# Performance work log

Hardware: AMD Instinct MI355X
Metric: run time of the kernel (lower is better)

Reference implementation:

```python
import jax, jax.numpy as jnp
import numpy as np

NUM_NODES = 50000
NUM_OBS = 800000


def graph_conv(x, src, dst, ew, W_rel, b_rel, W_root):
    # PyG GraphConv: out[i] = lin_rel(sum_{j->i} e * x[j]) + lin_root(x[i])
    msg = x[src] * ew[:, None]                         # [E, d_in] gather + weight
    agg = jax.ops.segment_sum(msg, dst, num_segments=NUM_NODES)  # scatter-add
    return agg @ W_rel + b_rel + x @ W_root


def setup_inputs() -> dict:
    key = jax.random.key(0)
    ks = jax.random.split(key, 16)
    E = 2 * NUM_OBS
    def lin(k, i, o):
        return jax.random.normal(k, (i, o), jnp.float32) / np.sqrt(i)
    return {
        "x": jax.random.normal(ks[0], (NUM_NODES, 2), jnp.float32),
        "edge_index": jax.random.randint(ks[1], (2, E), 0, NUM_NODES, jnp.int32),
        "edge_weight_norm": jax.random.uniform(ks[2], (E,), jnp.float32),
        "num_obs": NUM_OBS,
        "W1_rel": lin(ks[3], 2, 128), "b1": jnp.zeros((128,), jnp.float32),
        "W1_root": lin(ks[4], 2, 128),
        "W2_rel": lin(ks[5], 128, 64), "b2": jnp.zeros((64,), jnp.float32),
        "W2_root": lin(ks[6], 128, 64),
        "W3_rel": lin(ks[7], 64, 64), "b3": jnp.zeros((64,), jnp.float32),
        "W3_root": lin(ks[8], 64, 64),
        "dec_W1": lin(ks[9], 128, 128), "dec_b1": jnp.zeros((128,), jnp.float32),
        "dec_W2": lin(ks[10], 128, 1), "dec_b2": jnp.zeros((1,), jnp.float32),
    }


def reference(x, edge_index, edge_weight_norm, num_obs,
              W1_rel, b1, W1_root, W2_rel, b2, W2_root, W3_rel, b3, W3_root,
              dec_W1, dec_b1, dec_W2, dec_b2):
    src, dst = edge_index[0], edge_index[1]
    # encoder (eval mode: dropout is identity)
    h = jax.nn.relu(graph_conv(x, src, dst, edge_weight_norm, W1_rel, b1, W1_root))
    h = jax.nn.relu(graph_conv(h, src, dst, edge_weight_norm, W2_rel, b2, W2_root))
    z = graph_conv(h, src, dst, edge_weight_norm, W3_rel, b3, W3_root)
    # decoder over the first num_obs edges
    s = src[:num_obs]
    d = dst[:num_obs]
    h_cat = jnp.concatenate([z[s], z[d]], axis=1)      # [num_obs, 2*latent]
    pred = (jax.nn.relu(h_cat @ dec_W1 + dec_b1) @ dec_W2 + dec_b2)[:, 0]
    # pred_full[:num_obs] = pred; pred_full[num_obs:2*num_obs] = pred
    pred_full = jnp.concatenate([pred, pred], axis=0)
    return pred_full, z
```

## Files before the change

kernel.cpp:

```cpp
#include <hip/hip_runtime.h>
#include <hip/hip_bf16.h>

static inline int cdiv(long long a, long long b) { return (int)((a + b - 1) / b); }

__device__ inline float bf_lo(unsigned u) { return __uint_as_float(u << 16); }
__device__ inline float bf_hi(unsigned u) { return __uint_as_float(u & 0xffff0000u); }

typedef short bf16x8 __attribute__((ext_vector_type(8)));
typedef float f32x4 __attribute__((ext_vector_type(4)));

#define CHUNK 8192

__global__ __launch_bounds__(256) void prep_weights_kernel(
    const float* __restrict__ W2rel, const float* __restrict__ W2rt,
    const float* __restrict__ W3rel, const float* __restrict__ W3rt,
    const float* __restrict__ dW1, __hip_bfloat16* __restrict__ wt)
{
    int i = blockIdx.x * 256 + threadIdx.x;
    if (i >= 40960) return;
    float v;
    if (i < 8192)       { int n = i >> 7, k = i & 127;              v = W2rel[k * 64 + n]; }
    else if (i < 16384) { int j = i - 8192;  int n = j >> 7, k = j & 127; v = W2rt[k * 64 + n]; }
    else if (i < 20480) { int j = i - 16384; int n = j >> 6, k = j & 63;  v = W3rel[k * 64 + n]; }
    else if (i < 24576) { int j = i - 20480; int n = j >> 6, k = j & 63;  v = W3rt[k * 64 + n]; }
    else if (i < 32768) { int j = i - 24576; int n = j >> 6, k = j & 63;  v = dW1[k * 128 + n]; }
    else                { int j = i - 32768; int n = j >> 6, k = j & 63;  v = dW1[(64 + k) * 128 + n]; }
    wt[i] = __float2bfloat16(v);
}

template <int K, int NOUT, int EPI>
__global__ __launch_bounds__(256) void mfma_gemm_kernel(
    const __hip_bfloat16* __restrict__ A,
    const __hip_bfloat16* __restrict__ Wt,
    const float* __restrict__ bias,
    const float* __restrict__ extra,
    __hip_bfloat16* __restrict__ outb,
    float* __restrict__ outf, int M)
{
    constexpr int KF = K / 32;
    constexpr int SPW = NOUT / 64;
    const int wv = threadIdx.x >> 6;
    const int lane = threadIdx.x & 63;
    const int m = lane & 15, q = lane >> 4;
    const int row0 = blockIdx.x * 16;
    const int arow = row0 + m;

    bf16x8 af[KF];
    #pragma unroll
    for (int kf = 0; kf < KF; kf++)
        af[kf] = *(const bf16x8*)(A + (size_t)arow * K + kf * 32 + q * 8);

    #pragma unroll
    for (int s = 0; s < SPW; s++) {
        const int col = (wv * SPW + s) * 16 + m;
        f32x4 acc = {0.f, 0.f, 0.f, 0.f};
        #pragma unroll
        for (int kf = 0; kf < KF; kf++) {
            bf16x8 bf = *(const bf16x8*)(Wt + (size_t)col * K + kf * 32 + q * 8);
            acc = __builtin_amdgcn_mfma_f32_16x16x32_bf16(af[kf], bf, acc, 0, 0, 0);
        }
        #pragma unroll
        for (int r = 0; r < 4; r++) {
            int rr = row0 + q * 4 + r;
            size_t idx = (size_t)rr * NOUT + col;
            float v = acc[r];
            if (EPI >= 1) v += extra[idx] + bias[col];
            if (EPI == 1) v = fmaxf(v, 0.f);
            if (EPI == 2) outf[idx] = v;
            outb[idx] = __float2bfloat16(v);
        }
    }
}


__global__ __launch_bounds__(256) void p1_hist_kernel(
    const int* __restrict__ dst, int* __restrict__ ghist,
    int E, int nchunks, int nb)
{
    __shared__ int sh[512];
    int c = blockIdx.x;
    for (int i = threadIdx.x; i < nb; i += 256) sh[i] = 0;
    __syncthreads();
    int base = c * CHUNK;
    int end = min(base + CHUNK, E);
    for (int i = base + threadIdx.x; i < end; i += 256)
        atomicAdd(&sh[dst[i] >> 7], 1);
    __syncthreads();
    for (int i = threadIdx.x; i < nb; i += 256)
        ghist[i * nchunks + c] = sh[i];
}

__global__ __launch_bounds__(256) void p2_scatter_kernel(
    const int* __restrict__ src, const int* __restrict__ dst,
    const float* __restrict__ ew, const int* __restrict__ gs,
    uint2* __restrict__ bpos, int E, int nchunks, int nb)
{
    __shared__ int cur[512];
    int c = blockIdx.x;
    for (int i = threadIdx.x; i < nb; i += 256) cur[i] = gs[i * nchunks + c];
    __syncthreads();
    int base = c * CHUNK;
    int end = min(base + CHUNK, E);
    for (int i = base + threadIdx.x; i < end; i += 256) {
        int d = dst[i];
        int pos = atomicAdd(&cur[d >> 7], 1);
        bpos[pos] = make_uint2(((unsigned)d << 16) | (unsigned)src[i],
                               __float_as_uint(ew[i]));
    }
}

__global__ __launch_bounds__(256) void p3_place_kernel(
    const uint2* __restrict__ bpos, const int* __restrict__ gs,
    int* __restrict__ deg, int* __restrict__ off,
    float2* __restrict__ csr, int E, int nchunks, int nb, int N)
{
    __shared__ int cnt[128];
    __shared__ int pos[128];
    int b = blockIdx.x;
    int nodebase = b << 7;
    if (threadIdx.x < 128) cnt[threadIdx.x] = 0;
    __syncthreads();
    int begin = gs[b * nchunks];
    int bend = (b + 1 < nb) ? gs[(b + 1) * nchunks] : E;
    for (int i = begin + threadIdx.x; i < bend; i += 256)
        atomicAdd(&cnt[(bpos[i].x >> 16) - nodebase], 1);
    __syncthreads();
    int v = 0;
    if (threadIdx.x < 128) { v = cnt[threadIdx.x]; pos[threadIdx.x] = v; }
    __syncthreads();
    #pragma unroll
    for (int ofs = 1; ofs < 128; ofs <<= 1) {
        int t = 0;
        if (threadIdx.x < 128 && threadIdx.x >= ofs) t = pos[threadIdx.x - ofs];
        __syncthreads();
        if (threadIdx.x < 128) pos[threadIdx.x] += t;
        __syncthreads();
    }
    if (threadIdx.x < 128) {
        int ex = begin + pos[threadIdx.x] - v;
        int n = nodebase + threadIdx.x;
        if (n < N) { off[n] = ex; deg[n] = v; }
        cnt[threadIdx.x] = ex;
    }
    __syncthreads();
    for (int i = begin + threadIdx.x; i < bend; i += 256) {
        uint2 en = bpos[i];
        int d = en.x >> 16;
        int p = atomicAdd(&cnt[d - nodebase], 1);
        csr[p] = make_float2(__int_as_float((int)(en.x & 0xffffu)),
                             __uint_as_float(en.y));
    }
}


__global__ __launch_bounds__(1024) void scan_block_kernel(
    const int* __restrict__ in, int* __restrict__ out,
    int* __restrict__ partials, int N)
{
    __shared__ int sdata[1024];
    const int tid = threadIdx.x;
    const int i = blockIdx.x * 1024 + tid;
    int v = (i < N) ? in[i] : 0;
    sdata[tid] = v;
    __syncthreads();
    #pragma unroll
    for (int ofs = 1; ofs < 1024; ofs <<= 1) {
        int t = (tid >= ofs) ? sdata[tid - ofs] : 0;
        __syncthreads();
        sdata[tid] += t;
        __syncthreads();
    }
    if (i < N) out[i] = sdata[tid] - v;
    if (partials && tid == 1023) partials[blockIdx.x] = sdata[1023];
}

__global__ __launch_bounds__(1024) void scan_add_kernel(
    int* __restrict__ off, const int* __restrict__ blockoff, int N)
{
    int i = blockIdx.x * blockDim.x + threadIdx.x;
    if (i < N) off[i] += blockoff[i >> 10];
}


__global__ __launch_bounds__(256) void hist_kernel(
    const int* __restrict__ dst, int* __restrict__ deg, int E)
{
    int e = blockIdx.x * blockDim.x + threadIdx.x;
    if (e < E) atomicAdd(&deg[dst[e]], 1);
}

__global__ __launch_bounds__(256) void fill_csr_kernel(
    const int* __restrict__ src, const int* __restrict__ dst,
    const float* __restrict__ ew, const int* __restrict__ off,
    int* __restrict__ cursor, float2* __restrict__ csr, int E)
{
    int e = blockIdx.x * blockDim.x + threadIdx.x;
    if (e >= E) return;
    int d = dst[e];
    int i = off[d] + atomicAdd(&cursor[d], 1);
    csr[i] = make_float2(__int_as_float(src[e]), ew[e]);
}


__global__ __launch_bounds__(256) void layer1_fused_kernel(
    const float2* __restrict__ x2, const float2* __restrict__ csr,
    const int* __restrict__ off, const int* __restrict__ deg,
    const float* __restrict__ W1rel, const float* __restrict__ W1rt,
    const float* __restrict__ b1, __hip_bfloat16* __restrict__ h1b, int N)
{
    int t = blockIdx.x * blockDim.x + threadIdx.x;
    int n = t >> 6;
    if (n >= N) return;
    int lane = t & 63;
    int beg = off[n], cnt = deg[n];
    float a0 = 0.f, a1 = 0.f;
    for (int i = lane; i < cnt; i += 64) {
        float2 c = csr[beg + i];
        float2 xs = x2[__float_as_int(c.x)];
        a0 = fmaf(c.y, xs.x, a0);
        a1 = fmaf(c.y, xs.y, a1);
    }
    #pragma unroll
    for (int o = 32; o > 0; o >>= 1) {
        a0 += __shfl_xor(a0, o, 64);
        a1 += __shfl_xor(a1, o, 64);
    }
    float2 xn = x2[n];
    float v0 = b1[lane] + a0 * W1rel[lane] + a1 * W1rel[128 + lane]
             + xn.x * W1rt[lane] + xn.y * W1rt[128 + lane];
    float v1 = b1[64 + lane] + a0 * W1rel[64 + lane] + a1 * W1rel[192 + lane]
             + xn.x * W1rt[64 + lane] + xn.y * W1rt[192 + lane];
    h1b[(size_t)n * 128 + lane]      = __float2bfloat16(fmaxf(v0, 0.f));
    h1b[(size_t)n * 128 + 64 + lane] = __float2bfloat16(fmaxf(v1, 0.f));
}


__global__ __launch_bounds__(256) void gather_b16_kernel(
    const float2* __restrict__ csr, const int* __restrict__ off,
    const int* __restrict__ deg, const __hip_bfloat162* __restrict__ p,
    float* __restrict__ agg, int N)
{
    int t = blockIdx.x * blockDim.x + threadIdx.x;
    int n = t >> 6;
    if (n >= N) return;
    int lane = t & 63;
    int half = lane >> 5;
    int fp = lane & 31;
    int beg = off[n], cnt = deg[n];
    float a0 = 0.f, a1 = 0.f;
    int i = half;
    for (; i + 2 < cnt; i += 4) {
        float2 c0 = csr[beg + i];
        float2 c1 = csr[beg + i + 2];
        float2 v0 = __bfloat1622float2(p[(size_t)__float_as_int(c0.x) * 32 + fp]);
        float2 v1 = __bfloat1622float2(p[(size_t)__float_as_int(c1.x) * 32 + fp]);
        a0 = fmaf(c0.y, v0.x, a0); a1 = fmaf(c0.y, v0.y, a1);
        a0 = fmaf(c1.y, v1.x, a0); a1 = fmaf(c1.y, v1.y, a1);
    }
    for (; i < cnt; i += 2) {
        float2 c = csr[beg + i];
        float2 v = __bfloat1622float2(p[(size_t)__float_as_int(c.x) * 32 + fp]);
        a0 = fmaf(c.y, v.x, a0); a1 = fmaf(c.y, v.y, a1);
    }
    a0 += __shfl_xor(a0, 32, 64);
    a1 += __shfl_xor(a1, 32, 64);
    if (half == 0)
        ((float2*)agg)[(size_t)n * 32 + fp] = make_float2(a0, a1);
}


__global__ __launch_bounds__(256) void scatter_f64_kernel(
    const int* __restrict__ src, const int* __restrict__ dst,
    const float* __restrict__ ew, const float* __restrict__ p,
    float* __restrict__ agg, int E)
{
    int t = blockIdx.x * blockDim.x + threadIdx.x;
    int e = t >> 6;
    if (e >= E) return;
    int j = t & 63;
    atomicAdd(&agg[(size_t)dst[e] * 64 + j], p[(size_t)src[e] * 64 + j] * ew[e]);
}

__global__ __launch_bounds__(256) void scatter_f2_kernel(
    const int* __restrict__ src, const int* __restrict__ dst,
    const float* __restrict__ ew, const float* __restrict__ x,
    float* __restrict__ agg, int E)
{
    int e = blockIdx.x * blockDim.x + threadIdx.x;
    if (e >= E) return;
    int s = src[e], d = dst[e];
    float w = ew[e];
    atomicAdd(&agg[d * 2 + 0], x[s * 2 + 0] * w);
    atomicAdd(&agg[d * 2 + 1], x[s * 2 + 1] * w);
}

__global__ __launch_bounds__(256) void layer1_kernel(
    const float* __restrict__ x, const float* __restrict__ agg,
    const float* __restrict__ W1rel, const float* __restrict__ W1root,
    const float* __restrict__ b1, float* __restrict__ h1, int N)
{
    int t = blockIdx.x * blockDim.x + threadIdx.x;
    if (t >= N * 128) return;
    int n = t >> 7, j = t & 127;
    float v = b1[j]
        + agg[n * 2 + 0] * W1rel[j] + agg[n * 2 + 1] * W1rel[128 + j]
        + x[n * 2 + 0] * W1root[j] + x[n * 2 + 1] * W1root[128 + j];
    h1[t] = fmaxf(v, 0.f);
}

template <int K, int NOUT, bool RELU, bool HAS_EXTRA, bool HAS_BIAS, bool OUT_BF16>
__global__ __launch_bounds__(256) void gemm_small(
    const float* __restrict__ in, int M,
    const float* __restrict__ W, int ldw, int woff,
    const float* __restrict__ bias,
    const float* __restrict__ extra,
    void* __restrict__ out_)
{
    constexpr int CPT = NOUT / 64;
    __shared__ float sW[K * NOUT];
    __shared__ float sX[4][K];
    const int tid = threadIdx.x;
    const int lane = tid & 63;
    const int wv = tid >> 6;
    for (int idx = tid; idx < K * NOUT; idx += 256) {
        int k = idx / NOUT;
        int j = idx - k * NOUT;
        sW[idx] = W[(size_t)(k + woff) * ldw + j];
    }
    __syncthreads();
    const int ROWS = 32;
    int r0 = blockIdx.x * ROWS;
    for (int rr = wv; rr < ROWS; rr += 4) {
        int r = r0 + rr;
        if (r >= M) break;
        #pragma unroll
        for (int kk = lane; kk < K; kk += 64) sX[wv][kk] = in[(size_t)r * K + kk];
        float acc[CPT][4];
        #pragma unroll
        for (int c = 0; c < CPT; c++)
            #pragma unroll
            for (int u = 0; u < 4; u++) acc[c][u] = 0.f;
        #pragma unroll
        for (int k = 0; k < K; k += 4) {
            #pragma unroll
            for (int u = 0; u < 4; u++) {
                float xv = sX[wv][k + u];
                #pragma unroll
                for (int c = 0; c < CPT; c++)
                    acc[c][u] = fmaf(xv, sW[(k + u) * NOUT + c * 64 + lane], acc[c][u]);
            }
        }
        #pragma unroll
        for (int c = 0; c < CPT; c++) {
            float v = (acc[c][0] + acc[c][1]) + (acc[c][2] + acc[c][3]);
            int j = c * 64 + lane;
            if (HAS_EXTRA) v += extra[(size_t)r * NOUT + j];
            if (HAS_BIAS) v += bias[j];
            if (RELU) v = fmaxf(v, 0.f);
            if (OUT_BF16)
                ((__hip_bfloat16*)out_)[(size_t)r * NOUT + j] = __float2bfloat16(v);
            else
                ((float*)out_)[(size_t)r * NOUT + j] = v;
        }
    }
}


__global__ __launch_bounds__(256) void decoder16_kernel(
    const int* __restrict__ src, const int* __restrict__ dst,
    const uint4* __restrict__ Za, const uint4* __restrict__ Zb,
    const float* __restrict__ db1, const float* __restrict__ dW2,
    const float* __restrict__ db2, float* __restrict__ pred,
    int Eobs, int nseg)
{
    int t = blockIdx.x * blockDim.x + threadIdx.x;
    int l = t & 15;
    int seg = t >> 4;
    float4 c1a = ((const float4*)db1)[2 * l];
    float4 c1b = ((const float4*)db1)[2 * l + 1];
    float4 w2a = ((const float4*)dW2)[2 * l];
    float4 w2b = ((const float4*)dW2)[2 * l + 1];
    float b2v = db2[0];

    for (int e = seg; e < Eobs; e += nseg) {
        int s = src[e], d = dst[e];
        uint4 ua = Za[(size_t)s * 16 + l];
        uint4 ub = Zb[(size_t)d * 16 + l];
        float acc;
        acc  = fmaxf(bf_lo(ua.x) + bf_lo(ub.x) + c1a.x, 0.f) * w2a.x;
        acc += fmaxf(bf_hi(ua.x) + bf_hi(ub.x) + c1a.y, 0.f) * w2a.y;
        acc += fmaxf(bf_lo(ua.y) + bf_lo(ub.y) + c1a.z, 0.f) * w2a.z;
        acc += fmaxf(bf_hi(ua.y) + bf_hi(ub.y) + c1a.w, 0.f) * w2a.w;
        acc += fmaxf(bf_lo(ua.z) + bf_lo(ub.z) + c1b.x, 0.f) * w2b.x;
        acc += fmaxf(bf_hi(ua.z) + bf_hi(ub.z) + c1b.y, 0.f) * w2b.y;
        acc += fmaxf(bf_lo(ua.w) + bf_lo(ub.w) + c1b.z, 0.f) * w2b.z;
        acc += fmaxf(bf_hi(ua.w) + bf_hi(ub.w) + c1b.w, 0.f) * w2b.w;
        #pragma unroll
        for (int o = 8; o > 0; o >>= 1) acc += __shfl_xor(acc, o, 64);
        if (l == 0) {
            float pv = acc + b2v;
            pred[e] = pv;
            pred[e + Eobs] = pv;
        }
    }
}

__global__ __launch_bounds__(256) void decoder_kernel(
    const int* __restrict__ src, const int* __restrict__ dst,
    const float* __restrict__ Z1a, const float* __restrict__ Z1b,
    const float* __restrict__ db1, const float* __restrict__ dW2,
    const float* __restrict__ db2, float* __restrict__ pred, int Eobs)
{
    int t = blockIdx.x * blockDim.x + threadIdx.x;
    int e = t >> 6;
    if (e >= Eobs) return;
    int lane = threadIdx.x & 63;
    int s = src[e], d = dst[e];
    float t0 = Z1a[(size_t)s * 128 + lane] + Z1b[(size_t)d * 128 + lane] + db1[lane];
    float t1 = Z1a[(size_t)s * 128 + lane + 64] + Z1b[(size_t)d * 128 + lane + 64] + db1[lane + 64];
    t0 = fmaxf(t0, 0.f);
    t1 = fmaxf(t1, 0.f);
    float acc = t0 * dW2[lane] + t1 * dW2[lane + 64];
    #pragma unroll
    for (int off = 32; off > 0; off >>= 1) acc += __shfl_xor(acc, off, 64);
    if (lane == 0) {
        float pv = acc + db2[0];
        pred[e] = pv;
        pred[e + Eobs] = pv;
    }
}


extern "C" void kernel_launch(void* const* d_in, const int* in_sizes, int n_in,
                              void* d_out, int out_size, void* d_ws, size_t ws_size,
                              hipStream_t stream)
{
    const float* x     = (const float*)d_in[0];
    const int*   ei    = (const int*)d_in[1];
    const float* ew    = (const float*)d_in[2];
    const float* W1rel = (const float*)d_in[4];
    const float* b1    = (const float*)d_in[5];
    const float* W1rt  = (const float*)d_in[6];
    const float* W2rel = (const float*)d_in[7];
    const float* b2    = (const float*)d_in[8];
    const float* W2rt  = (const float*)d_in[9];
    const float* W3rel = (const float*)d_in[10];
    const float* b3    = (const float*)d_in[11];
    const float* W3rt  = (const float*)d_in[12];
    const float* dW1   = (const float*)d_in[13];
    const float* db1   = (const float*)d_in[14];
    const float* dW2   = (const float*)d_in[15];
    const float* db2   = (const float*)d_in[16];

    const int E    = in_sizes[2];
    const int N    = in_sizes[0] / 2;
    const int Eobs = E / 2;
    const int* src = ei;
    const int* dst = ei + E;

    float* agg  = (float*)d_ws;
    float* R1   = agg + (size_t)N * 64;
    float* R2   = R1 + (size_t)N * 64;
    float* R3   = R2 + (size_t)N * 32;
    float* R4   = R3 + (size_t)N * 32;
    int*   deg  = (int*)(R4 + (size_t)N * 64);
    int*   off  = deg + N;
    int*   par1 = off + N;
    int*   par2 = par1 + 1024;
    float* wtf  = (float*)(par2 + 1024);
    __hip_bfloat16* wt = (__hip_bfloat16*)wtf;
    float2* csr = (float2*)(wtf + 20480);

    __hip_bfloat16* h1b   = (__hip_bfloat16*)R1;
    __hip_bfloat16* Z1a16 = (__hip_bfloat16*)R1;
    __hip_bfloat16* pb16  = (__hip_bfloat16*)R2;
    __hip_bfloat16* zb16  = (__hip_bfloat16*)R2;
    __hip_bfloat16* h2b   = (__hip_bfloat16*)R3;
    __hip_bfloat16* Z1b16 = (__hip_bfloat16*)R4;
    uint2* bpos  = (uint2*)R4;
    int*   ghist = (int*)agg;

    const int nb      = (N + 127) >> 7;
    const int nchunks = cdiv(E, CHUNK);
    const int M       = nb * nchunks;
    int* ghist_s = ghist + M;

    size_t need = ((size_t)N * 258 + 22528 + (size_t)E * 2) * 4;
    const bool fast = (ws_size >= need) && nb <= 512 && N <= 65535 &&
                      (N % 16 == 0) &&
                      (size_t)E * 2 <= (size_t)N * 64 &&
                      (size_t)M * 2 <= (size_t)N * 64;

    float* pred = (float*)d_out;
    float* z    = pred + E;

    const int nscanM = cdiv(M, 1024);
    const int gblocks = N / 16;

    __hip_bfloat16* wt2rel = wt;
    __hip_bfloat16* wt2rt  = wt + 8192;
    __hip_bfloat16* wt3rel = wt + 16384;
    __hip_bfloat16* wt3rt  = wt + 20480;
    __hip_bfloat16* wtd1a  = wt + 24576;
    __hip_bfloat16* wtd1b  = wt + 32768;

    if (fast) {
        prep_weights_kernel<<<160, 256, 0, stream>>>(W2rel, W2rt, W3rel, W3rt, dW1, wt);

        p1_hist_kernel<<<nchunks, 256, 0, stream>>>(dst, ghist, E, nchunks, nb);
        scan_block_kernel<<<nscanM, 1024, 0, stream>>>(ghist, ghist_s, par1, M);
        scan_block_kernel<<<1, 1024, 0, stream>>>(par1, par2, nullptr, nscanM);
        scan_add_kernel<<<cdiv(M, 1024), 1024, 0, stream>>>(ghist_s, par2, M);
        p2_scatter_kernel<<<nchunks, 256, 0, stream>>>(src, dst, ew, ghist_s, bpos, E, nchunks, nb);
        p3_place_kernel<<<nb, 256, 0, stream>>>(bpos, ghist_s, deg, off, csr, E, nchunks, nb, N);

        layer1_fused_kernel<<<cdiv((long long)N * 64, 256), 256, 0, stream>>>(
            (const float2*)x, csr, off, deg, W1rel, W1rt, b1, h1b, N);

        mfma_gemm_kernel<128, 64, 0><<<gblocks, 256, 0, stream>>>(
            h1b, wt2rel, nullptr, nullptr, pb16, nullptr, N);
        gather_b16_kernel<<<cdiv((long long)N * 64, 256), 256, 0, stream>>>(
            csr, off, deg, (const __hip_bfloat162*)pb16, agg, N);
        mfma_gemm_kernel<128, 64, 1><<<gblocks, 256, 0, stream>>>(
            h1b, wt2rt, b2, agg, h2b, nullptr, N);

        mfma_gemm_kernel<64, 64, 0><<<gblocks, 256, 0, stream>>>(
            h2b, wt3rel, nullptr, nullptr, pb16, nullptr, N);
        gather_b16_kernel<<<cdiv((long long)N * 64, 256), 256, 0, stream>>>(
            csr, off, deg, (const __hip_bfloat162*)pb16, agg, N);
        mfma_gemm_kernel<64, 64, 2><<<gblocks, 256, 0, stream>>>(
            h2b, wt3rt, b3, agg, zb16, z, N);

        mfma_gemm_kernel<64, 128, 0><<<gblocks, 256, 0, stream>>>(
            zb16, wtd1a, nullptr, nullptr, Z1a16, nullptr, N);
        mfma_gemm_kernel<64, 128, 0><<<gblocks, 256, 0, stream>>>(
            zb16, wtd1b, nullptr, nullptr, Z1b16, nullptr, N);
        int dblocks = 2048;
        if (dblocks > cdiv((long long)Eobs * 16, 256)) dblocks = cdiv((long long)Eobs * 16, 256);
        int nseg = dblocks * 16;
        decoder16_kernel<<<dblocks, 256, 0, stream>>>(
            src, dst, (const uint4*)Z1a16, (const uint4*)Z1b16,
            db1, dW2, db2, pred, Eobs, nseg);
    } else {
        float* h1   = agg + (size_t)N * 64;
        float* h2   = h1 + (size_t)N * 128;
        float* pbuf = h2 + (size_t)N * 64;
        float* Z1a = h1;
        float* Z1b = h2;
        hipMemsetAsync(agg, 0, (size_t)N * 2 * sizeof(float), stream);
        scatter_f2_kernel<<<cdiv(E, 256), 256, 0, stream>>>(src, dst, ew, x, agg, E);
        layer1_kernel<<<cdiv((long long)N * 128, 256), 256, 0, stream>>>(x, agg, W1rel, W1rt, b1, h1, N);

        gemm_small<128, 64, false, false, false, false><<<cdiv(N, 32), 256, 0, stream>>>(
            h1, N, W2rel, 64, 0, nullptr, nullptr, pbuf);
        hipMemsetAsync(agg, 0, (size_t)N * 64 * sizeof(float), stream);
        scatter_f64_kernel<<<cdiv((long long)E * 64, 256), 256, 0, stream>>>(src, dst, ew, pbuf, agg, E);
        gemm_small<128, 64, true, true, true, false><<<cdiv(N, 32), 256, 0, stream>>>(
            h1, N, W2rt, 64, 0, b2, agg, h2);

        gemm_small<64, 64, false, false, false, false><<<cdiv(N, 32), 256, 0, stream>>>(
            h2, N, W3rel, 64, 0, nullptr, nullptr, pbuf);
        hipMemsetAsync(agg, 0, (size_t)N * 64 * sizeof(float), stream);
        scatter_f64_kernel<<<cdiv((long long)E * 64, 256), 256, 0, stream>>>(src, dst, ew, pbuf, agg, E);
        gemm_small<64, 64, false, true, true, false><<<cdiv(N, 32), 256, 0, stream>>>(
            h2, N, W3rt, 64, 0, b3, agg, z);

        gemm_small<64, 128, false, false, false, false><<<cdiv(N, 32), 256, 0, stream>>>(
            z, N, dW1, 128, 0, nullptr, nullptr, Z1a);
        gemm_small<64, 128, false, false, false, false><<<cdiv(N, 32), 256, 0, stream>>>(
            z, N, dW1, 128, 64, nullptr, nullptr, Z1b);
        decoder_kernel<<<cdiv((long long)Eobs * 64, 256), 256, 0, stream>>>(
            src, dst, Z1a, Z1b, db1, dW2, db2, pred, Eobs);
    }
}
```

Baseline: 397.1 us.

## Fuse gather into root GEMM, pack CSR to 4 bytes, merge prep kernels

Folds the neighbor gather-aggregation into the root-weight MFMA GEMM epilogue, so the fp32 agg buffer is no longer written and re-read. Packs each CSR entry into 32 bits (16-bit src index plus a bf16 edge weight) to halve CSR traffic. Merges the histogram and weight-prep kernels into one launch and the two decoder GEMMs into one. Edge weights now round to bf16, costing some precision, and the src index is limited to 16 bits.

Measured after the change: 391.2 us. About the same (-1.5%).

```diff
diff --git a/kernel.cpp b/kernel.cpp
--- a/kernel.cpp
+++ b/kernel.cpp
@@ -11,31 +11,173 @@
 
 #define CHUNK 8192
 
-__global__ __launch_bounds__(256) void prep_weights_kernel(
+__global__ __launch_bounds__(256) void p1_prep_kernel(
+    const int* __restrict__ dst, int* __restrict__ ghist,
+    int E, int nchunks, int nb,
     const float* __restrict__ W2rel, const float* __restrict__ W2rt,
     const float* __restrict__ W3rel, const float* __restrict__ W3rt,
     const float* __restrict__ dW1, __hip_bfloat16* __restrict__ wt)
 {
-    int i = blockIdx.x * 256 + threadIdx.x;
-    if (i >= 40960) return;
-    float v;
-    if (i < 8192)       { int n = i >> 7, k = i & 127;              v = W2rel[k * 64 + n]; }
-    else if (i < 16384) { int j = i - 8192;  int n = j >> 7, k = j & 127; v = W2rt[k * 64 + n]; }
-    else if (i < 20480) { int j = i - 16384; int n = j >> 6, k = j & 63;  v = W3rel[k * 64 + n]; }
-    else if (i < 24576) { int j = i - 20480; int n = j >> 6, k = j & 63;  v = W3rt[k * 64 + n]; }
-    else if (i < 32768) { int j = i - 24576; int n = j >> 6, k = j & 63;  v = dW1[k * 128 + n]; }
-    else                { int j = i - 32768; int n = j >> 6, k = j & 63;  v = dW1[(64 + k) * 128 + n]; }
-    wt[i] = __float2bfloat16(v);
-}
-
-template <int K, int NOUT, int EPI>
+    __shared__ int sh[512];
+    if (blockIdx.x < (unsigned)nchunks) {
+        int c = blockIdx.x;
+        for (int i = threadIdx.x; i < nb; i += 256) sh[i] = 0;
+        __syncthreads();
+        int base = c * CHUNK;
+        int end = min(base + CHUNK, E);
+        for (int i = base + threadIdx.x; i < end; i += 256)
+            atomicAdd(&sh[dst[i] >> 7], 1);
+        __syncthreads();
+        for (int i = threadIdx.x; i < nb; i += 256)
+            ghist[i * nchunks + c] = sh[i];
+    } else {
+        int i = (blockIdx.x - nchunks) * 256 + threadIdx.x;
+        if (i >= 40960) return;
+        float v;
+        if (i < 8192)       { int n = i >> 7, k = i & 127;               v = W2rel[k * 64 + n]; }
+        else if (i < 16384) { int j = i - 8192;  int n = j >> 7, k = j & 127; v = W2rt[k * 64 + n]; }
+        else if (i < 20480) { int j = i - 16384; int n = j >> 6, k = j & 63;  v = W3rel[k * 64 + n]; }
+        else if (i < 24576) { int j = i - 20480; int n = j >> 6, k = j & 63;  v = W3rt[k * 64 + n]; }
+        else if (i < 32768) { int j = i - 24576; int n = j >> 6, k = j & 63;  v = dW1[k * 128 + n]; }
+        else                { int j = i - 32768; int n = j >> 6, k = j & 63;  v = dW1[(64 + k) * 128 + n]; }
+        wt[i] = __float2bfloat16(v);
+    }
+}
+
+
+__global__ __launch_bounds__(256) void p2_scatter_kernel(
+    const int* __restrict__ src, const int* __restrict__ dst,
+    const float* __restrict__ ew, const int* __restrict__ gs,
+    uint2* __restrict__ bpos, int E, int nchunks, int nb)
+{
+    __shared__ int cur[512];
+    int c = blockIdx.x;
+    for (int i = threadIdx.x; i < nb; i += 256) cur[i] = gs[i * nchunks + c];
+    __syncthreads();
+    int base = c * CHUNK;
+    int end = min(base + CHUNK, E);
+    for (int i = base + threadIdx.x; i < end; i += 256) {
+        int d = dst[i];
+        int pos = atomicAdd(&cur[d >> 7], 1);
+        bpos[pos] = make_uint2(((unsigned)d << 16) | (unsigned)src[i],
+                               __float_as_uint(ew[i]));
+    }
+}
+
+
+__global__ __launch_bounds__(256) void p3_place_kernel(
+    const uint2* __restrict__ bpos, const int* __restrict__ gs,
+    int* __restrict__ deg, int* __restrict__ off,
+    unsigned* __restrict__ csr4, int E, int nchunks, int nb, int N)
+{
+    __shared__ int cnt[128];
+    __shared__ int pos[128];
+    int b = blockIdx.x;
+    int nodebase = b << 7;
+    if (threadIdx.x < 128) cnt[threadIdx.x] = 0;
+    __syncthreads();
+    int begin = gs[b * nchunks];
+    int bend = (b + 1 < nb) ? gs[(b + 1) * nchunks] : E;
+    for (int i = begin + threadIdx.x; i < bend; i += 256)
+        atomicAdd(&cnt[(bpos[i].x >> 16) - nodebase], 1);
+    __syncthreads();
+    int v = 0;
+    if (threadIdx.x < 128) { v = cnt[threadIdx.x]; pos[threadIdx.x] = v; }
+    __syncthreads();
+    #pragma unroll
+    for (int ofs = 1; ofs < 128; ofs <<= 1) {
+        int t = 0;
+        if (threadIdx.x < 128 && threadIdx.x >= ofs) t = pos[threadIdx.x - ofs];
+        __syncthreads();
+        if (threadIdx.x < 128) pos[threadIdx.x] += t;
+        __syncthreads();
+    }
+    if (threadIdx.x < 128) {
+        int ex = begin + pos[threadIdx.x] - v;
+        int n = nodebase + threadIdx.x;
+        if (n < N) { off[n] = ex; deg[n] = v; }
+        cnt[threadIdx.x] = ex;
+    }
+    __syncthreads();
+    for (int i = begin + threadIdx.x; i < bend; i += 256) {
+        uint2 en = bpos[i];
+        int d = en.x >> 16;
+        int p = atomicAdd(&cnt[d - nodebase], 1);
+        unsigned u = en.y;
+        unsigned wb = (u + 0x7fffu + ((u >> 16) & 1u)) & 0xffff0000u;
+        csr4[p] = wb | (en.x & 0xffffu);
+    }
+}
+
+
+__global__ __launch_bounds__(1024) void scan_block_kernel(
+    const int* __restrict__ in, int* __restrict__ out,
+    int* __restrict__ partials, int N)
+{
+    __shared__ int sdata[1024];
+    const int tid = threadIdx.x;
+    const int i = blockIdx.x * 1024 + tid;
+    int v = (i < N) ? in[i] : 0;
+    sdata[tid] = v;
+    __syncthreads();
+    #pragma unroll
+    for (int ofs = 1; ofs < 1024; ofs <<= 1) {
+        int t = (tid >= ofs) ? sdata[tid - ofs] : 0;
+        __syncthreads();
+        sdata[tid] += t;
+        __syncthreads();
+    }
+    if (i < N) out[i] = sdata[tid] - v;
+    if (partials && tid == 1023) partials[blockIdx.x] = sdata[1023];
+}
+
+__global__ __launch_bounds__(1024) void scan_add_kernel(
+    int* __restrict__ off, const int* __restrict__ blockoff, int N)
+{
+    int i = blockIdx.x * blockDim.x + threadIdx.x;
+    if (i < N) off[i] += blockoff[i >> 10];
+}
+
+
+__global__ __launch_bounds__(256) void layer1_fused_kernel(
+    const float2* __restrict__ x2, const unsigned* __restrict__ csr4,
+    const int* __restrict__ off, const int* __restrict__ deg,
+    const float* __restrict__ W1rel, const float* __restrict__ W1rt,
+    const float* __restrict__ b1, __hip_bfloat16* __restrict__ h1b, int N)
+{
+    int t = blockIdx.x * blockDim.x + threadIdx.x;
+    int n = t >> 6;
+    if (n >= N) return;
+    int lane = t & 63;
+    int beg = off[n], cnt = deg[n];
+    float a0 = 0.f, a1 = 0.f;
+    for (int i = lane; i < cnt; i += 64) {
+        unsigned c = csr4[beg + i];
+        float w = bf_hi(c);
+        float2 xs = x2[c & 0xffffu];
+        a0 = fmaf(w, xs.x, a0);
+        a1 = fmaf(w, xs.y, a1);
+    }
+    #pragma unroll
+    for (int o = 32; o > 0; o >>= 1) {
+        a0 += __shfl_xor(a0, o, 64);
+        a1 += __shfl_xor(a1, o, 64);
+    }
+    float2 xn = x2[n];
+    float v0 = b1[lane] + a0 * W1rel[lane] + a1 * W1rel[128 + lane]
+             + xn.x * W1rt[lane] + xn.y * W1rt[128 + lane];
+    float v1 = b1[64 + lane] + a0 * W1rel[64 + lane] + a1 * W1rel[192 + lane]
+             + xn.x * W1rt[64 + lane] + xn.y * W1rt[192 + lane];
+    h1b[(size_t)n * 128 + lane]      = __float2bfloat16(fmaxf(v0, 0.f));
+    h1b[(size_t)n * 128 + 64 + lane] = __float2bfloat16(fmaxf(v1, 0.f));
+}
+
+
+template <int K, int NOUT>
 __global__ __launch_bounds__(256) void mfma_gemm_kernel(
     const __hip_bfloat16* __restrict__ A,
     const __hip_bfloat16* __restrict__ Wt,
-    const float* __restrict__ bias,
-    const float* __restrict__ extra,
-    __hip_bfloat16* __restrict__ outb,
-    float* __restrict__ outf, int M)
+    __hip_bfloat16* __restrict__ outb, int M)
 {
     constexpr int KF = K / 32;
     constexpr int SPW = NOUT / 64;
@@ -62,305 +204,119 @@
         #pragma unroll
         for (int r = 0; r < 4; r++) {
             int rr = row0 + q * 4 + r;
-            size_t idx = (size_t)rr * NOUT + col;
-            float v = acc[r];
-            if (EPI >= 1) v += extra[idx] + bias[col];
-            if (EPI == 1) v = fmaxf(v, 0.f);
-            if (EPI == 2) outf[idx] = v;
-            outb[idx] = __float2bfloat16(v);
-        }
-    }
-}
-
-
-__global__ __launch_bounds__(256) void p1_hist_kernel(
-    const int* __restrict__ dst, int* __restrict__ ghist,
-    int E, int nchunks, int nb)
-{
-    __shared__ int sh[512];
-    int c = blockIdx.x;
-    for (int i = threadIdx.x; i < nb; i += 256) sh[i] = 0;
-    __syncthreads();
-    int base = c * CHUNK;
-    int end = min(base + CHUNK, E);
-    for (int i = base + threadIdx.x; i < end; i += 256)
-        atomicAdd(&sh[dst[i] >> 7], 1);
-    __syncthreads();
-    for (int i = threadIdx.x; i < nb; i += 256)
-        ghist[i * nchunks + c] = sh[i];
-}
-
-__global__ __launch_bounds__(256) void p2_scatter_kernel(
-    const int* __restrict__ src, const int* __restrict__ dst,
-    const float* __restrict__ ew, const int* __restrict__ gs,
-    uint2* __restrict__ bpos, int E, int nchunks, int nb)
-{
-    __shared__ int cur[512];
-    int c = blockIdx.x;
-    for (int i = threadIdx.x; i < nb; i += 256) cur[i] = gs[i * nchunks + c];
-    __syncthreads();
-    int base = c * CHUNK;
-    int end = min(base + CHUNK, E);
-    for (int i = base + threadIdx.x; i < end; i += 256) {
-        int d = dst[i];
-        int pos = atomicAdd(&cur[d >> 7], 1);
-        bpos[pos] = make_uint2(((unsigned)d << 16) | (unsigned)src[i],
-                               __float_as_uint(ew[i]));
-    }
-}
-
-__global__ __launch_bounds__(256) void p3_place_kernel(
-    const uint2* __restrict__ bpos, const int* __restrict__ gs,
-    int* __restrict__ deg, int* __restrict__ off,
-    float2* __restrict__ csr, int E, int nchunks, int nb, int N)
-{
-    __shared__ int cnt[128];
-    __shared__ int pos[128];
-    int b = blockIdx.x;
-    int nodebase = b << 7;
-    if (threadIdx.x < 128) cnt[threadIdx.x] = 0;
-    __syncthreads();
-    int begin = gs[b * nchunks];
-    int bend = (b + 1 < nb) ? gs[(b + 1) * nchunks] : E;
-    for (int i = begin + threadIdx.x; i < bend; i += 256)
-        atomicAdd(&cnt[(bpos[i].x >> 16) - nodebase], 1);
-    __syncthreads();
-    int v = 0;
-    if (threadIdx.x < 128) { v = cnt[threadIdx.x]; pos[threadIdx.x] = v; }
-    __syncthreads();
-    #pragma unroll
-    for (int ofs = 1; ofs < 128; ofs <<= 1) {
-        int t = 0;
-        if (threadIdx.x < 128 && threadIdx.x >= ofs) t = pos[threadIdx.x - ofs];
-        __syncthreads();
-        if (threadIdx.x < 128) pos[threadIdx.x] += t;
-        __syncthreads();
-    }
-    if (threadIdx.x < 128) {
-        int ex = begin + pos[threadIdx.x] - v;
-        int n = nodebase + threadIdx.x;
-        if (n < N) { off[n] = ex; deg[n] = v; }
-        cnt[threadIdx.x] = ex;
-    }
-    __syncthreads();
-    for (int i = begin + threadIdx.x; i < bend; i += 256) {
-        uint2 en = bpos[i];
-        int d = en.x >> 16;
-        int p = atomicAdd(&cnt[d - nodebase], 1);
-        csr[p] = make_float2(__int_as_float((int)(en.x & 0xffffu)),
-                             __uint_as_float(en.y));
-    }
-}
-
-
-__global__ __launch_bounds__(1024) void scan_block_kernel(
-    const int* __restrict__ in, int* __restrict__ out,
-    int* __restrict__ partials, int N)
-{
-    __shared__ int sdata[1024];
-    const int tid = threadIdx.x;
-    const int i = blockIdx.x * 1024 + tid;
-    int v = (i < N) ? in[i] : 0;
-    sdata[tid] = v;
-    __syncthreads();
-    #pragma unroll
-    for (int ofs = 1; ofs < 1024; ofs <<= 1) {
-        int t = (tid >= ofs) ? sdata[tid - ofs] : 0;
-        __syncthreads();
-        sdata[tid] += t;
-        __syncthreads();
-    }
-    if (i < N) out[i] = sdata[tid] - v;
-    if (partials && tid == 1023) partials[blockIdx.x] = sdata[1023];
-}
-
-__global__ __launch_bounds__(1024) void scan_add_kernel(
-    int* __restrict__ off, const int* __restrict__ blockoff, int N)
-{
-    int i = blockIdx.x * blockDim.x + threadIdx.x;
-    if (i < N) off[i] += blockoff[i >> 10];
-}
-
-
-__global__ __launch_bounds__(256) void hist_kernel(
-    const int* __restrict__ dst, int* __restrict__ deg, int E)
-{
-    int e = blockIdx.x * blockDim.x + threadIdx.x;
-    if (e < E) atomicAdd(&deg[dst[e]], 1);
-}
-
-__global__ __launch_bounds__(256) void fill_csr_kernel(
-    const int* __restrict__ src, const int* __restrict__ dst,
-    const float* __restrict__ ew, const int* __restrict__ off,
-    int* __restrict__ cursor, float2* __restrict__ csr, int E)
-{
-    int e = blockIdx.x * blockDim.x + threadIdx.x;
-    if (e >= E) return;
-    int d = dst[e];
-    int i = off[d] + atomicAdd(&cursor[d], 1);
-    csr[i] = make_float2(__int_as_float(src[e]), ew[e]);
-}
-
-
-__global__ __launch_bounds__(256) void layer1_fused_kernel(
-    const float2* __restrict__ x2, const float2* __restrict__ csr,
-    const int* __restrict__ off, const int* __restrict__ deg,
-    const float* __restrict__ W1rel, const float* __restrict__ W1rt,
-    const float* __restrict__ b1, __hip_bfloat16* __restrict__ h1b, int N)
-{
-    int t = blockIdx.x * blockDim.x + threadIdx.x;
-    int n = t >> 6;
-    if (n >= N) return;
-    int lane = t & 63;
-    int beg = off[n], cnt = deg[n];
-    float a0 = 0.f, a1 = 0.f;
-    for (int i = lane; i < cnt; i += 64) {
-        float2 c = csr[beg + i];
-        float2 xs = x2[__float_as_int(c.x)];
-        a0 = fmaf(c.y, xs.x, a0);
-        a1 = fmaf(c.y, xs.y, a1);
-    }
-    #pragma unroll
-    for (int o = 32; o > 0; o >>= 1) {
-        a0 += __shfl_xor(a0, o, 64);
-        a1 += __shfl_xor(a1, o, 64);
-    }
-    float2 xn = x2[n];
-    float v0 = b1[lane] + a0 * W1rel[lane] + a1 * W1rel[128 + lane]
-             + xn.x * W1rt[lane] + xn.y * W1rt[128 + lane];
-    float v1 = b1[64 + lane] + a0 * W1rel[64 + lane] + a1 * W1rel[192 + lane]
-             + xn.x * W1rt[64 + lane] + xn.y * W1rt[192 + lane];
-    h1b[(size_t)n * 128 + lane]      = __float2bfloat16(fmaxf(v0, 0.f));
-    h1b[(size_t)n * 128 + 64 + lane] = __float2bfloat16(fmaxf(v1, 0.f));
-}
-
-
-__global__ __launch_bounds__(256) void gather_b16_kernel(
-    const float2* __restrict__ csr, const int* __restrict__ off,
-    const int* __restrict__ deg, const __hip_bfloat162* __restrict__ p,
-    float* __restrict__ agg, int N)
-{
-    int t = blockIdx.x * blockDim.x + threadIdx.x;
-    int n = t >> 6;
-    if (n >= N) return;
-    int lane = t & 63;
-    int half = lane >> 5;
-    int fp = lane & 31;
-    int beg = off[n], cnt = deg[n];
-    float a0 = 0.f, a1 = 0.f;
-    int i = half;
-    for (; i + 2 < cnt; i += 4) {
-        float2 c0 = csr[beg + i];
-        float2 c1 = csr[beg + i + 2];
-        float2 v0 = __bfloat1622float2(p[(size_t)__float_as_int(c0.x) * 32 + fp]);
-        float2 v1 = __bfloat1622float2(p[(size_t)__float_as_int(c1.x) * 32 + fp]);
-        a0 = fmaf(c0.y, v0.x, a0); a1 = fmaf(c0.y, v0.y, a1);
-        a0 = fmaf(c1.y, v1.x, a0); a1 = fmaf(c1.y, v1.y, a1);
-    }
-    for (; i < cnt; i += 2) {
-        float2 c = csr[beg + i];
-        float2 v = __bfloat1622float2(p[(size_t)__float_as_int(c.x) * 32 + fp]);
-        a0 = fmaf(c.y, v.x, a0); a1 = fmaf(c.y, v.y, a1);
-    }
-    a0 += __shfl_xor(a0, 32, 64);
-    a1 += __shfl_xor(a1, 32, 64);
-    if (half == 0)
-        ((float2*)agg)[(size_t)n * 32 + fp] = make_float2(a0, a1);
-}
-
-
-__global__ __launch_bounds__(256) void scatter_f64_kernel(
-    const int* __restrict__ src, const int* __restrict__ dst,
-    const float* __restrict__ ew, const float* __restrict__ p,
-    float* __restrict__ agg, int E)
-{
-    int t = blockIdx.x * blockDim.x + threadIdx.x;
-    int e = t >> 6;
-    if (e >= E) return;
-    int j = t & 63;
-    atomicAdd(&agg[(size_t)dst[e] * 64 + j], p[(size_t)src[e] * 64 + j] * ew[e]);
-}
-
-__global__ __launch_bounds__(256) void scatter_f2_kernel(
-    const int* __restrict__ src, const int* __restrict__ dst,
-    const float* __restrict__ ew, const float* __restrict__ x,
-    float* __restrict__ agg, int E)
-{
-    int e = blockIdx.x * blockDim.x + threadIdx.x;
-    if (e >= E) return;
-    int s = src[e], d = dst[e];
-    float w = ew[e];
-    atomicAdd(&agg[d * 2 + 0], x[s * 2 + 0] * w);
-    atomicAdd(&agg[d * 2 + 1], x[s * 2 + 1] * w);
-}
-
-__global__ __launch_bounds__(256) void layer1_kernel(
-    const float* __restrict__ x, const float* __restrict__ agg,
-    const float* __restrict__ W1rel, const float* __restrict__ W1root,
-    const float* __restrict__ b1, float* __restrict__ h1, int N)
-{
-    int t = blockIdx.x * blockDim.x + threadIdx.x;
-    if (t >= N * 128) return;
-    int n = t >> 7, j = t & 127;
-    float v = b1[j]
-        + agg[n * 2 + 0] * W1rel[j] + agg[n * 2 + 1] * W1rel[128 + j]
-        + x[n * 2 + 0] * W1root[j] + x[n * 2 + 1] * W1root[128 + j];
-    h1[t] = fmaxf(v, 0.f);
-}
-
-template <int K, int NOUT, bool RELU, bool HAS_EXTRA, bool HAS_BIAS, bool OUT_BF16>
-__global__ __launch_bounds__(256) void gemm_small(
-    const float* __restrict__ in, int M,
-    const float* __restrict__ W, int ldw, int woff,
+            outb[(size_t)rr * NOUT + col] = __float2bfloat16(acc[r]);
+        }
+    }
+}
+
+
+template <int K, int EPI>
+__global__ __launch_bounds__(256) void mfma_root_kernel(
+    const __hip_bfloat16* __restrict__ A,
+    const __hip_bfloat16* __restrict__ Wt,
     const float* __restrict__ bias,
-    const float* __restrict__ extra,
-    void* __restrict__ out_)
-{
-    constexpr int CPT = NOUT / 64;
-    __shared__ float sW[K * NOUT];
-    __shared__ float sX[4][K];
-    const int tid = threadIdx.x;
-    const int lane = tid & 63;
-    const int wv = tid >> 6;
-    for (int idx = tid; idx < K * NOUT; idx += 256) {
-        int k = idx / NOUT;
-        int j = idx - k * NOUT;
-        sW[idx] = W[(size_t)(k + woff) * ldw + j];
-    }
-    __syncthreads();
-    const int ROWS = 32;
-    int r0 = blockIdx.x * ROWS;
-    for (int rr = wv; rr < ROWS; rr += 4) {
-        int r = r0 + rr;
-        if (r >= M) break;
-        #pragma unroll
-        for (int kk = lane; kk < K; kk += 64) sX[wv][kk] = in[(size_t)r * K + kk];
-        float acc[CPT][4];
-        #pragma unroll
-        for (int c = 0; c < CPT; c++)
-            #pragma unroll
-            for (int u = 0; u < 4; u++) acc[c][u] = 0.f;
-        #pragma unroll
-        for (int k = 0; k < K; k += 4) {
-            #pragma unroll
-            for (int u = 0; u < 4; u++) {
-                float xv = sX[wv][k + u];
-                #pragma unroll
-                for (int c = 0; c < CPT; c++)
-                    acc[c][u] = fmaf(xv, sW[(k + u) * NOUT + c * 64 + lane], acc[c][u]);
-            }
-        }
-        #pragma unroll
-        for (int c = 0; c < CPT; c++) {
-            float v = (acc[c][0] + acc[c][1]) + (acc[c][2] + acc[c][3]);
-            int j = c * 64 + lane;
-            if (HAS_EXTRA) v += extra[(size_t)r * NOUT + j];
-            if (HAS_BIAS) v += bias[j];
-            if (RELU) v = fmaxf(v, 0.f);
-            if (OUT_BF16)
-                ((__hip_bfloat16*)out_)[(size_t)r * NOUT + j] = __float2bfloat16(v);
-            else
-                ((float*)out_)[(size_t)r * NOUT + j] = v;
+    const unsigned* __restrict__ csr4, const int* __restrict__ off,
+    const int* __restrict__ deg,
+    const __hip_bfloat162* __restrict__ p,
+    __hip_bfloat16* __restrict__ outb, float* __restrict__ outf, int M)
+{
+    __shared__ float aggL[16][64];
+    constexpr int KF = K / 32;
+    const int wv = threadIdx.x >> 6;
+    const int lane = threadIdx.x & 63;
+    const int half = lane >> 5, fp = lane & 31;
+    const int row0 = blockIdx.x * 16;
+
+    #pragma unroll
+    for (int nn = 0; nn < 4; nn++) {
+        int n = row0 + wv * 4 + nn;
+        int beg = off[n], cnt = deg[n];
+        float a0 = 0.f, a1 = 0.f;
+        int i = half;
+        for (; i + 2 < cnt; i += 4) {
+            unsigned c0 = csr4[beg + i];
+            unsigned c1 = csr4[beg + i + 2];
+            float2 v0 = __bfloat1622float2(p[(size_t)(c0 & 0xffffu) * 32 + fp]);
+            float2 v1 = __bfloat1622float2(p[(size_t)(c1 & 0xffffu) * 32 + fp]);
+            float w0 = bf_hi(c0), w1 = bf_hi(c1);
+            a0 = fmaf(w0, v0.x, a0); a1 = fmaf(w0, v0.y, a1);
+            a0 = fmaf(w1, v1.x, a0); a1 = fmaf(w1, v1.y, a1);
+        }
+        for (; i < cnt; i += 2) {
+            unsigned c = csr4[beg + i];
+            float2 v = __bfloat1622float2(p[(size_t)(c & 0xffffu) * 32 + fp]);
+            float w = bf_hi(c);
+            a0 = fmaf(w, v.x, a0); a1 = fmaf(w, v.y, a1);
+        }
+        a0 += __shfl_xor(a0, 32, 64);
+        a1 += __shfl_xor(a1, 32, 64);
+        if (half == 0) {
+            aggL[wv * 4 + nn][2 * fp]     = a0;
+            aggL[wv * 4 + nn][2 * fp + 1] = a1;
+        }
+    }
+    __syncthreads();
+
+    const int m = lane & 15, q = lane >> 4;
+    const int arow = row0 + m;
+    bf16x8 af[KF];
+    #pragma unroll
+    for (int kf = 0; kf < KF; kf++)
+        af[kf] = *(const bf16x8*)(A + (size_t)arow * K + kf * 32 + q * 8);
+    const int col = wv * 16 + m;
+    f32x4 acc = {0.f, 0.f, 0.f, 0.f};
+    #pragma unroll
+    for (int kf = 0; kf < KF; kf++) {
+        bf16x8 bf = *(const bf16x8*)(Wt + (size_t)col * K + kf * 32 + q * 8);
+        acc = __builtin_amdgcn_mfma_f32_16x16x32_bf16(af[kf], bf, acc, 0, 0, 0);
+    }
+    #pragma unroll
+    for (int r = 0; r < 4; r++) {
+        int rloc = q * 4 + r;
+        size_t idx = (size_t)(row0 + rloc) * 64 + col;
+        float v = acc[r] + aggL[rloc][col] + bias[col];
+        if (EPI == 1) v = fmaxf(v, 0.f);
+        if (EPI == 2) outf[idx] = v;
+        outb[idx] = __float2bfloat16(v);
+    }
+}
+
+
+__global__ __launch_bounds__(256) void dec_gemm_kernel(
+    const __hip_bfloat16* __restrict__ A,
+    const __hip_bfloat16* __restrict__ Wt0,
+    const __hip_bfloat16* __restrict__ Wt1,
+    __hip_bfloat16* __restrict__ out0,
+    __hip_bfloat16* __restrict__ out1, int gblocks)
+{
+    constexpr int K = 64, KF = 2, SPW = 2;
+    const int hb = (blockIdx.x >= (unsigned)gblocks) ? 1 : 0;
+    const __hip_bfloat16* Wt = hb ? Wt1 : Wt0;
+    __hip_bfloat16* outb = hb ? out1 : out0;
+    const int wv = threadIdx.x >> 6;
+    const int lane = threadIdx.x & 63;
+    const int m = lane & 15, q = lane >> 4;
+    const int row0 = (blockIdx.x - hb * gblocks) * 16;
+    const int arow = row0 + m;
+
+    bf16x8 af[KF];
+    #pragma unroll
+    for (int kf = 0; kf < KF; kf++)
+        af[kf] = *(const bf16x8*)(A + (size_t)arow * K + kf * 32 + q * 8);
+
+    #pragma unroll
+    for (int s = 0; s < SPW; s++) {
+        const int col = (wv * SPW + s) * 16 + m;
+        f32x4 acc = {0.f, 0.f, 0.f, 0.f};
+        #pragma unroll
+        for (int kf = 0; kf < KF; kf++) {
+            bf16x8 bf = *(const bf16x8*)(Wt + (size_t)col * K + kf * 32 + q * 8);
+            acc = __builtin_amdgcn_mfma_f32_16x16x32_bf16(af[kf], bf, acc, 0, 0, 0);
+        }
+        #pragma unroll
+        for (int r = 0; r < 4; r++) {
+            int rr = row0 + q * 4 + r;
+            outb[(size_t)rr * 128 + col] = __float2bfloat16(acc[r]);
         }
     }
 }
@@ -401,6 +357,100 @@
             float pv = acc + b2v;
             pred[e] = pv;
             pred[e + Eobs] = pv;
+        }
+    }
+}
+
+
+__global__ __launch_bounds__(256) void scatter_f64_kernel(
+    const int* __restrict__ src, const int* __restrict__ dst,
+    const float* __restrict__ ew, const float* __restrict__ p,
+    float* __restrict__ agg, int E)
+{
+    int t = blockIdx.x * blockDim.x + threadIdx.x;
+    int e = t >> 6;
+    if (e >= E) return;
+    int j = t & 63;
+    atomicAdd(&agg[(size_t)dst[e] * 64 + j], p[(size_t)src[e] * 64 + j] * ew[e]);
+}
+
+__global__ __launch_bounds__(256) void scatter_f2_kernel(
+    const int* __restrict__ src, const int* __restrict__ dst,
+    const float* __restrict__ ew, const float* __restrict__ x,
+    float* __restrict__ agg, int E)
+{
+    int e = blockIdx.x * blockDim.x + threadIdx.x;
+    if (e >= E) return;
+    int s = src[e], d = dst[e];
+    float w = ew[e];
+    atomicAdd(&agg[d * 2 + 0], x[s * 2 + 0] * w);
+    atomicAdd(&agg[d * 2 + 1], x[s * 2 + 1] * w);
+}
+
+__global__ __launch_bounds__(256) void layer1_kernel(
+    const float* __restrict__ x, const float* __restrict__ agg,
+    const float* __restrict__ W1rel, const float* __restrict__ W1root,
+    const float* __restrict__ b1, float* __restrict__ h1, int N)
+{
+    int t = blockIdx.x * blockDim.x + threadIdx.x;
+    if (t >= N * 128) return;
+    int n = t >> 7, j = t & 127;
+    float v = b1[j]
+        + agg[n * 2 + 0] * W1rel[j] + agg[n * 2 + 1] * W1rel[128 + j]
+        + x[n * 2 + 0] * W1root[j] + x[n * 2 + 1] * W1root[128 + j];
+    h1[t] = fmaxf(v, 0.f);
+}
+
+template <int K, int NOUT, bool RELU, bool HAS_EXTRA, bool HAS_BIAS>
+__global__ __launch_bounds__(256) void gemm_small(
+    const float* __restrict__ in, int M,
+    const float* __restrict__ W, int ldw, int woff,
+    const float* __restrict__ bias,
+    const float* __restrict__ extra,
+    float* __restrict__ out)
+{
+    constexpr int CPT = NOUT / 64;
+    __shared__ float sW[K * NOUT];
+    __shared__ float sX[4][K];
+    const int tid = threadIdx.x;
+    const int lane = tid & 63;
+    const int wv = tid >> 6;
+    for (int idx = tid; idx < K * NOUT; idx += 256) {
+        int k = idx / NOUT;
+        int j = idx - k * NOUT;
+        sW[idx] = W[(size_t)(k + woff) * ldw + j];
+    }
+    __syncthreads();
+    const int ROWS = 32;
+    int r0 = blockIdx.x * ROWS;
+    for (int rr = wv; rr < ROWS; rr += 4) {
+        int r = r0 + rr;
+        if (r >= M) break;
+        #pragma unroll
+        for (int kk = lane; kk < K; kk += 64) sX[wv][kk] = in[(size_t)r * K + kk];
+        float acc[CPT][4];
+        #pragma unroll
+        for (int c = 0; c < CPT; c++)
+            #pragma unroll
+            for (int u = 0; u < 4; u++) acc[c][u] = 0.f;
+        #pragma unroll
+        for (int k = 0; k < K; k += 4) {
+            #pragma unroll
+            for (int u = 0; u < 4; u++) {
+                float xv = sX[wv][k + u];
+                #pragma unroll
+                for (int c = 0; c < CPT; c++)
+                    acc[c][u] = fmaf(xv, sW[(k + u) * NOUT + c * 64 + lane], acc[c][u]);
+            }
+        }
+        #pragma unroll
+        for (int c = 0; c < CPT; c++) {
+            float v = (acc[c][0] + acc[c][1]) + (acc[c][2] + acc[c][3]);
+            int j = c * 64 + lane;
+            if (HAS_EXTRA) v += extra[(size_t)r * NOUT + j];
+            if (HAS_BIAS) v += bias[j];
+            if (RELU) v = fmaxf(v, 0.f);
+            out[(size_t)r * NOUT + j] = v;
         }
     }
 }
@@ -458,8 +508,8 @@
     const int* src = ei;
     const int* dst = ei + E;
 
-    float* agg  = (float*)d_ws;
-    float* R1   = agg + (size_t)N * 64;
+    float* R0   = (float*)d_ws;
+    float* R1   = R0 + (size_t)N * 64;
     float* R2   = R1 + (size_t)N * 64;
     float* R3   = R2 + (size_t)N * 32;
     float* R4   = R3 + (size_t)N * 32;
@@ -469,16 +519,16 @@
     int*   par2 = par1 + 1024;
     float* wtf  = (float*)(par2 + 1024);
     __hip_bfloat16* wt = (__hip_bfloat16*)wtf;
-    float2* csr = (float2*)(wtf + 20480);
-
+    unsigned* csr4 = (unsigned*)(wtf + 20480);
+
+    __hip_bfloat16* zb16  = (__hip_bfloat16*)R0;
     __hip_bfloat16* h1b   = (__hip_bfloat16*)R1;
     __hip_bfloat16* Z1a16 = (__hip_bfloat16*)R1;
     __hip_bfloat16* pb16  = (__hip_bfloat16*)R2;
-    __hip_bfloat16* zb16  = (__hip_bfloat16*)R2;
     __hip_bfloat16* h2b   = (__hip_bfloat16*)R3;
     __hip_bfloat16* Z1b16 = (__hip_bfloat16*)R4;
     uint2* bpos  = (uint2*)R4;
-    int*   ghist = (int*)agg;
+    int*   ghist = (int*)R0;
 
     const int nb      = (N + 127) >> 7;
     const int nchunks = cdiv(E, CHUNK);
@@ -505,36 +555,29 @@
     __hip_bfloat16* wtd1b  = wt + 32768;
 
     if (fast) {
-        prep_weights_kernel<<<160, 256, 0, stream>>>(W2rel, W2rt, W3rel, W3rt, dW1, wt);
-
-        p1_hist_kernel<<<nchunks, 256, 0, stream>>>(dst, ghist, E, nchunks, nb);
+        p1_prep_kernel<<<nchunks + 160, 256, 0, stream>>>(
+            dst, ghist, E, nchunks, nb, W2rel, W2rt, W3rel, W3rt, dW1, wt);
         scan_block_kernel<<<nscanM, 1024, 0, stream>>>(ghist, ghist_s, par1, M);
         scan_block_kernel<<<1, 1024, 0, stream>>>(par1, par2, nullptr, nscanM);
         scan_add_kernel<<<cdiv(M, 1024), 1024, 0, stream>>>(ghist_s, par2, M);
         p2_scatter_kernel<<<nchunks, 256, 0, stream>>>(src, dst, ew, ghist_s, bpos, E, nchunks, nb);
-        p3_place_kernel<<<nb, 256, 0, stream>>>(bpos, ghist_s, deg, off, csr, E, nchunks, nb, N);
+        p3_place_kernel<<<nb, 256, 0, stream>>>(bpos, ghist_s, deg, off, csr4, E, nchunks, nb, N);
 
         layer1_fused_kernel<<<cdiv((long long)N * 64, 256), 256, 0, stream>>>(
-            (const float2*)x, csr, off, deg, W1rel, W1rt, b1, h1b, N);
-
-        mfma_gemm_kernel<128, 64, 0><<<gblocks, 256, 0, stream>>>(
-            h1b, wt2rel, nullptr, nullptr, pb16, nullptr, N);
-        gather_b16_kernel<<<cdiv((long long)N * 64, 256), 256, 0, stream>>>(
-            csr, off, deg, (const __hip_bfloat162*)pb16, agg, N);
-        mfma_gemm_kernel<128, 64, 1><<<gblocks, 256, 0, stream>>>(
-            h1b, wt2rt, b2, agg, h2b, nullptr, N);
-
-        mfma_gemm_kernel<64, 64, 0><<<gblocks, 256, 0, stream>>>(
-            h2b, wt3rel, nullptr, nullptr, pb16, nullptr, N);
-        gather_b16_kernel<<<cdiv((long long)N * 64, 256), 256, 0, stream>>>(
-            csr, off, deg, (const __hip_bfloat162*)pb16, agg, N);
-        mfma_gemm_kernel<64, 64, 2><<<gblocks, 256, 0, stream>>>(
-            h2b, wt3rt, b3, agg, zb16, z, N);
-
-        mfma_gemm_kernel<64, 128, 0><<<gblocks, 256, 0, stream>>>(
-            zb16, wtd1a, nullptr, nullptr, Z1a16, nullptr, N);
-        mfma_gemm_kernel<64, 128, 0><<<gblocks, 256, 0, stream>>>(
-            zb16, wtd1b, nullptr, nullptr, Z1b16, nullptr, N);
+            (const float2*)x, csr4, off, deg, W1rel, W1rt, b1, h1b, N);
+
+        mfma_gemm_kernel<128, 64><<<gblocks, 256, 0, stream>>>(h1b, wt2rel, pb16, N);
+        mfma_root_kernel<128, 1><<<gblocks, 256, 0, stream>>>(
+            h1b, wt2rt, b2, csr4, off, deg, (const __hip_bfloat162*)pb16,
+            h2b, nullptr, N);
+
+        mfma_gemm_kernel<64, 64><<<gblocks, 256, 0, stream>>>(h2b, wt3rel, pb16, N);
+        mfma_root_kernel<64, 2><<<gblocks, 256, 0, stream>>>(
+            h2b, wt3rt, b3, csr4, off, deg, (const __hip_bfloat162*)pb16,
+            zb16, z, N);
+
+        dec_gemm_kernel<<<2 * gblocks, 256, 0, stream>>>(
+            zb16, wtd1a, wtd1b, Z1a16, Z1b16, gblocks);
         int dblocks = 2048;
         if (dblocks > cdiv((long long)Eobs * 16, 256)) dblocks = cdiv((long long)Eobs * 16, 256);
         int nseg = dblocks * 16;
@@ -542,6 +585,7 @@
             src, dst, (const uint4*)Z1a16, (const uint4*)Z1b16,
             db1, dW2, db2, pred, Eobs, nseg);
     } else {
+        float* agg  = R0;
         float* h1   = agg + (size_t)N * 64;
         float* h2   = h1 + (size_t)N * 128;
         float* pbuf = h2 + (size_t)N * 64;
@@ -551,23 +595,23 @@
         scatter_f2_kernel<<<cdiv(E, 256), 256, 0, stream>>>(src, dst, ew, x, agg, E);
         layer1_kernel<<<cdiv((long long)N * 128, 256), 256, 0, stream>>>(x, agg, W1rel, W1rt, b1, h1, N);
 
-        gemm_small<128, 64, false, false, false, false><<<cdiv(N, 32), 256, 0, stream>>>(
+        gemm_small<128, 64, false, false, false><<<cdiv(N, 32), 256, 0, stream>>>(
             h1, N, W2rel, 64, 0, nullptr, nullptr, pbuf);
         hipMemsetAsync(agg, 0, (size_t)N * 64 * sizeof(float), stream);
         scatter_f64_kernel<<<cdiv((long long)E * 64, 256), 256, 0, stream>>>(src, dst, ew, pbuf, agg, E);
-        gemm_small<128, 64, true, true, true, false><<<cdiv(N, 32), 256, 0, stream>>>(
+        gemm_small<128, 64, true, true, true><<<cdiv(N, 32), 256, 0, stream>>>(
             h1, N, W2rt, 64, 0, b2, agg, h2);
 
-        gemm_small<64, 64, false, false, false, false><<<cdiv(N, 32), 256, 0, stream>>>(
+        gemm_small<64, 64, false, false, false><<<cdiv(N, 32), 256, 0, stream>>>(
             h2, N, W3rel, 64, 0, nullptr, nullptr, pbuf);
         hipMemsetAsync(agg, 0, (size_t)N * 64 * sizeof(float), stream);
         scatter_f64_kernel<<<cdiv((long long)E * 64, 256), 256, 0, stream>>>(src, dst, ew, pbuf, agg, E);
-        gemm_small<64, 64, false, true, true, false><<<cdiv(N, 32), 256, 0, stream>>>(
+        gemm_small<64, 64, false, true, true><<<cdiv(N, 32), 256, 0, stream>>>(
             h2, N, W3rt, 64, 0, b3, agg, z);
 
-        gemm_small<64, 128, false, false, false, false><<<cdiv(N, 32), 256, 0, stream>>>(
+        gemm_small<64, 128, false, false, false><<<cdiv(N, 32), 256, 0, stream>>>(
             z, N, dW1, 128, 0, nullptr, nullptr, Z1a);
-        gemm_small<64, 128, false, false, false, false><<<cdiv(N, 32), 256, 0, stream>>>(
+        gemm_small<64, 128, false, false, false><<<cdiv(N, 32), 256, 0, stream>>>(
             z, N, dW1, 128, 64, nullptr, nullptr, Z1b);
         decoder_kernel<<<cdiv((long long)Eobs * 64, 256), 256, 0, stream>>>(
             src, dst, Z1a, Z1b, db1, dW2, db2, pred, Eobs);
```
